# Performance work log

Measured on AMD Instinct MI355X. Metric: run time of the kernel, lower is better.

Reference implementation:

```python
import jax, jax.numpy as jnp
import numpy as np
import jax.scipy.linalg as jsl

# ---- module constants (mirror __init__ buffers) ----
T0, T1, DT = 0.0, 1.0, 1e-3
DIM, NSTEPS, M, TQ, B = 8, 2048, 64, 1024, 1
DS = (T1 - T0) / NSTEPS
STEPS = jnp.linspace(T0, T1, NSTEPS + 1)            # [S+1]
ZPTS = jnp.linspace(T0 + DT * 5.5, T1 - DT * 5.5, M)  # inducing points [M]
SQRT_DS = float(np.sqrt(DS))
SQRT_DT = float(np.sqrt(DT))


def _hurst(t, y0, W1, b1, W2, b2, Wc1, bc1, Wc2, bc2, dw, cw):
    # compute_hurst: sigmoid(driving_action(t)*dw + condition_net(y0)*cw)
    tc_in = t.reshape(-1, 1)                                             # [N,1]
    feat = jnp.concatenate([jnp.sin(tc_in), jnp.cos(tc_in), tc_in], -1)  # [N,3]
    tc = jax.nn.sigmoid(jnp.tanh(feat @ W1.T + b1) @ W2.T + b2)          # [N,dim]
    pc = jax.nn.sigmoid(jnp.tanh(y0 @ Wc1.T + bc1) @ Wc2.T + bc2)        # [1,dim]
    return jax.nn.sigmoid(tc * dw + pc * cw)                             # [N,dim]


def _safe_pow(x, a):
    # x**a for x>=0, with well-defined (zero) gradient at x==0
    mask = x > 0
    xs = jnp.where(mask, x, 1.0)
    return jnp.where(mask, xs ** a, 0.0)


def _compute_weight(t, y0, params, eps=1e-12):
    # compute_weight (Muniandy et al. weight); returns [S, N, dim]
    h = _hurst(t, y0, *params)[None]                              # [1,N,dim]
    d0 = jax.nn.relu(t[None, :] - STEPS[:-1, None])[..., None]    # [S,N,1]
    d1 = jax.nn.relu(t[None, :] - STEPS[1:, None])[..., None]     # [S,N,1]
    w = jnp.sqrt(_safe_pow(d0, 2.0 * h) - _safe_pow(d1, 2.0 * h) + eps)
    w = w / jnp.sqrt(2.0 * h * DS)
    return w / jnp.exp(jax.lax.lgamma(h + 0.5))


def _increment_weight(t, y0, params):
    # increment_weight: g_i / dt (finite difference of clamped weights)
    wa = jnp.maximum(_compute_weight(t, y0, params), 0.0)
    wb = jnp.maximum(_compute_weight(t + DT, y0, params), 0.0)
    return jnp.maximum((wb - wa) * SQRT_DS / DT, 0.0)             # [S,N,dim]


def _forward(t, y0, eps_z, W1, b1, W2, b2, Wc1, bc1, Wc2, bc2, dw, cw):
    params = (W1, b1, W2, b2, Wc1, bc1, Wc2, bc2, dw, cw)
    # --- precompute (inducing points) ---
    Kz = _increment_weight(ZPTS, y0, params)                # [S,M,dim]
    Kzz = jnp.einsum('smd,skd->dmk', Kz, Kz)                # [dim,M,M]
    Lz = jnp.linalg.cholesky(Kzz + 1e-6 * jnp.eye(M, dtype=Kzz.dtype))
    delta_Bz = jnp.einsum('dmk,dkb->dmb', Lz, eps_z)        # [dim,M,B]
    # --- forward (mean / sqrt(var)*sqrt(dt)) ---
    Kt = _increment_weight(t, y0, params)                   # [S,T,dim]
    Ktz = jnp.einsum('std,smd->dtm', Kt, Kz)                # [dim,T,M]
    alpha = jax.vmap(lambda L, b: jsl.cho_solve((L, True), b))(
        Lz, jnp.swapaxes(Ktz, -1, -2))                      # [dim,M,T]
    mean = jnp.einsum('dmt,dmb->dtb', alpha, delta_Bz)      # [dim,T,B]
    Ktt = jnp.einsum('std,sud->dtu', Kt, Kt)                # [dim,T,T]
    var = Ktt - jnp.einsum('dmt,dmu->dtu', alpha, alpha)    # [dim,T,T]
    std = jnp.sqrt(jnp.maximum(var, 1e-12)) * SQRT_DT
    return mean.reshape(-1, DIM), std.reshape(-1, DIM)


def setup_inputs() -> dict:
    key = jax.random.key(0)
    ks = jax.random.split(key, 12)
    return {
        't': jax.random.uniform(ks[0], (TQ,), jnp.float32, T0 + 0.05, T1 - 0.05),
        'y0': jax.random.normal(ks[1], (1, 1), jnp.float32),
        'eps_z': jax.random.normal(ks[2], (DIM, M, B), jnp.float32),
        'W1': jax.random.normal(ks[3], (10, 3), jnp.float32) * 0.3,
        'b1': jax.random.normal(ks[4], (10,), jnp.float32) * 0.1,
        'W2': jax.random.normal(ks[5], (DIM, 10), jnp.float32) * 0.3,
        'b2': jax.random.normal(ks[6], (DIM,), jnp.float32) * 0.1,
        'Wc1': jax.random.normal(ks[7], (10, 1), jnp.float32) * 0.3,
        'bc1': jax.random.normal(ks[8], (10,), jnp.float32) * 0.1,
        'Wc2': jax.random.normal(ks[9], (DIM, 10), jnp.float32) * 0.3,
        'bc2': jax.random.normal(ks[10], (DIM,), jnp.float32) * 0.1,
        'dw': jnp.array([0.5], jnp.float32),
        'cw': jnp.array([0.5], jnp.float32),
    }


def reference(t, y0, eps_z, W1, b1, W2, b2, Wc1, bc1, Wc2, bc2, dw, cw):
    return _forward(t, y0, eps_z, W1, b1, W2, b2, Wc1, bc1, Wc2, bc2, dw, cw)
```

## Files before the change

kernel.cpp:

```cpp
#include <hip/hip_runtime.h>
#include <cmath>

#define DIMN 8
#define SSTEPS 2048
#define MZ 64
#define TQN 1024
#define DS_F    4.8828125e-4f
#define DT_F    1.0e-3f
#define SCALE_F 22.09708691207961f
#define SQRTDT_F 0.031622776601683794f
#define LN2_F   0.6931471805599453f

typedef _Float16 f16x8 __attribute__((ext_vector_type(8)));
typedef float f32x4 __attribute__((ext_vector_type(4)));

__device__ __forceinline__ float sigmoidf_(float x) { return 1.f / (1.f + expf(-x)); }

__device__ __forceinline__ void gl_lds16(const _Float16* g, _Float16* l)
{
    __builtin_amdgcn_global_load_lds(
        (const __attribute__((address_space(1))) unsigned int*)g,
        (__attribute__((address_space(3))) unsigned int*)l, 16, 0, 0);
}

__global__ void coef_kernel(const float* __restrict__ t_in, const float* __restrict__ y0,
                            const float* __restrict__ W1, const float* __restrict__ b1,
                            const float* __restrict__ W2, const float* __restrict__ b2,
                            const float* __restrict__ Wc1, const float* __restrict__ bc1,
                            const float* __restrict__ Wc2, const float* __restrict__ bc2,
                            const float* __restrict__ dw, const float* __restrict__ cw,
                            float4* __restrict__ coef_t, float4* __restrict__ coef_z,
                            float* __restrict__ times_z)
{
    int gid = blockIdx.x * blockDim.x + threadIdx.x;
    if (gid >= TQN + MZ) return;
    bool isz = gid >= TQN;
    float tv;
    if (!isz) {
        tv = t_in[gid];
    } else {
        int j = gid - TQN;
        tv = 0.0055f + (float)j * (0.989f / 63.0f);
        times_z[j] = tv;
    }
    float y = y0[0];
    float hc[10];
    #pragma unroll
    for (int j = 0; j < 10; ++j) hc[j] = tanhf(y * Wc1[j] + bc1[j]);
    float pc[DIMN];
    #pragma unroll
    for (int d = 0; d < DIMN; ++d) {
        float s = bc2[d];
        #pragma unroll
        for (int j = 0; j < 10; ++j) s += hc[j] * Wc2[d * 10 + j];
        pc[d] = sigmoidf_(s);
    }
    float dww = dw[0], cww = cw[0];
    float4 outv[DIMN];
    for (int which = 0; which < 2; ++which) {
        float tt = (which == 0) ? tv : tv + DT_F;
        float st = sinf(tt), ct = cosf(tt);
        float hid[10];
        #pragma unroll
        for (int j = 0; j < 10; ++j)
            hid[j] = tanhf(st * W1[j * 3 + 0] + ct * W1[j * 3 + 1] + tt * W1[j * 3 + 2] + b1[j]);
        #pragma unroll
        for (int d = 0; d < DIMN; ++d) {
            float s = b2[d];
            #pragma unroll
            for (int j = 0; j < 10; ++j) s += hid[j] * W2[d * 10 + j];
            float tc = sigmoidf_(s);
            float h = sigmoidf_(tc * dww + pc[d] * cww);
            float e = 2.f * h;
            float c = rsqrtf(e * DS_F) / tgammaf(h + 0.5f);
            if (which == 0) { outv[d].x = e; outv[d].y = c; }
            else            { outv[d].z = e; outv[d].w = c; }
        }
    }
    float4* dst = isz ? (coef_z + (size_t)(gid - TQN) * DIMN) : (coef_t + (size_t)gid * DIMN);
    #pragma unroll
    for (int d = 0; d < DIMN; ++d) dst[d] = outv[d];
}

__device__ __forceinline__ void side_weights(float tt, float e, float c, int sbase,
                                             float (&w)[8])
{
    float xprev = tt - (float)sbase * DS_F;
    float pa = 0.f;
    if (xprev > 0.f) pa = __builtin_amdgcn_exp2f(e * __builtin_amdgcn_logf(xprev));
    #pragma unroll
    for (int k = 1; k <= 8; ++k) {
        float xk = tt - (float)(sbase + k) * DS_F;
        float D, pan;
        if (xk > 0.f) {
            float om = xk * __builtin_amdgcn_rcpf(xprev);
            float y2 = e * __builtin_amdgcn_logf(om);
            float wl = y2 * LN2_F;
            float em = wl * (1.f + wl * (0.5f + wl * (0.16666667f + wl * (0.041666668f + wl * 0.008333334f))));
            float g = -em;
            if (wl < -0.3f) g = 1.f - __builtin_amdgcn_exp2f(y2);
            D = pa * g;
            pan = pa - D;
        } else {
            D = pa;
            pan = 0.f;
        }
        w[k - 1] = __builtin_amdgcn_sqrtf(D + 1e-12f) * c;
        pa = pan;
        xprev = xk;
    }
}

__device__ __forceinline__ unsigned pack_hl(float v)
{
    _Float16 h = (_Float16)v;
    _Float16 l = (_Float16)(v - (float)h);
    unsigned short hu = __builtin_bit_cast(unsigned short, h);
    unsigned short lu = __builtin_bit_cast(unsigned short, l);
    return (unsigned)hu | ((unsigned)lu << 16);
}

__global__ __launch_bounds__(256) void kmat_t_kernel(const float* __restrict__ times,
                                                     const float4* __restrict__ coef,
                                                     _Float16* __restrict__ KThi,
                                                     _Float16* __restrict__ KTlo)
{
    int tid = threadIdx.x;
    int txx = tid & 31, sidx = tid >> 5;
    int t = blockIdx.x * 32 + txx;
    int sbase = blockIdx.y * 64 + sidx * 8;
    int d = blockIdx.z;
    __shared__ unsigned shhl[32][65];
    float tq = times[t];
    float4 cf = coef[(size_t)t * DIMN + d];
    float wa[8], wb[8];
    side_weights(tq,        cf.x, cf.y, sbase, wa);
    side_weights(tq + DT_F, cf.z, cf.w, sbase, wb);
    #pragma unroll
    for (int k = 0; k < 8; ++k) {
        float v = fmaxf(wb[k] - wa[k], 0.f) * SCALE_F;
        shhl[txx][sidx * 8 + k] = pack_hl(v);
    }
    __syncthreads();
    int tl = tid >> 3, sc = tid & 7;
    unsigned dwv[8];
    #pragma unroll
    for (int j = 0; j < 8; ++j) dwv[j] = shhl[tl][sc * 8 + j];
    uint4 hv, lv;
    hv.x = __builtin_amdgcn_perm(dwv[1], dwv[0], 0x05040100u);
    hv.y = __builtin_amdgcn_perm(dwv[3], dwv[2], 0x05040100u);
    hv.z = __builtin_amdgcn_perm(dwv[5], dwv[4], 0x05040100u);
    hv.w = __builtin_amdgcn_perm(dwv[7], dwv[6], 0x05040100u);
    lv.x = __builtin_amdgcn_perm(dwv[1], dwv[0], 0x07060302u);
    lv.y = __builtin_amdgcn_perm(dwv[3], dwv[2], 0x07060302u);
    lv.z = __builtin_amdgcn_perm(dwv[5], dwv[4], 0x07060302u);
    lv.w = __builtin_amdgcn_perm(dwv[7], dwv[6], 0x07060302u);
    size_t o = ((size_t)(d * 1024) + blockIdx.x * 32 + tl) * 2048 + blockIdx.y * 64 + sc * 8;
    *(uint4*)&KThi[o] = hv;
    *(uint4*)&KTlo[o] = lv;
}

__global__ __launch_bounds__(256) void kmat_z_kernel(const float* __restrict__ times,
                                                     const float4* __restrict__ coef,
                                                     float* __restrict__ Kz,
                                                     _Float16* __restrict__ KzThi,
                                                     _Float16* __restrict__ KzTlo)
{
    int tid = threadIdx.x;
    int txx = tid & 31, sidx = tid >> 5;
    int m = blockIdx.x * 32 + txx;
    int sbase = blockIdx.y * 64 + sidx * 8;
    int d = blockIdx.z;
    __shared__ unsigned shhl[32][65];
    float tq = times[m];
    float4 cf = coef[(size_t)m * DIMN + d];
    float wa[8], wb[8];
    side_weights(tq,        cf.x, cf.y, sbase, wa);
    side_weights(tq + DT_F, cf.z, cf.w, sbase, wb);
    #pragma unroll
    for (int k = 0; k < 8; ++k) {
        float v = fmaxf(wb[k] - wa[k], 0.f) * SCALE_F;
        Kz[((size_t)d * SSTEPS + sbase + k) * 64 + m] = v;
        shhl[txx][sidx * 8 + k] = pack_hl(v);
    }
    __syncthreads();
    int tl = tid >> 3, sc = tid & 7;
    unsigned dwv[8];
    #pragma unroll
    for (int j = 0; j < 8; ++j) dwv[j] = shhl[tl][sc * 8 + j];
    uint4 hv, lv;
    hv.x = __builtin_amdgcn_perm(dwv[1], dwv[0], 0x05040100u);
    hv.y = __builtin_amdgcn_perm(dwv[3], dwv[2], 0x05040100u);
    hv.z = __builtin_amdgcn_perm(dwv[5], dwv[4], 0x05040100u);
    hv.w = __builtin_amdgcn_perm(dwv[7], dwv[6], 0x05040100u);
    lv.x = __builtin_amdgcn_perm(dwv[1], dwv[0], 0x07060302u);
    lv.y = __builtin_amdgcn_perm(dwv[3], dwv[2], 0x07060302u);
    lv.z = __builtin_amdgcn_perm(dwv[5], dwv[4], 0x07060302u);
    lv.w = __builtin_amdgcn_perm(dwv[7], dwv[6], 0x07060302u);
    size_t o = ((size_t)(d * 64) + blockIdx.x * 32 + tl) * 2048 + blockIdx.y * 64 + sc * 8;
    *(uint4*)&KzThi[o] = hv;
    *(uint4*)&KzTlo[o] = lv;
}

__global__ __launch_bounds__(256) void kzz_partial_kernel(const float* __restrict__ Kz,
                                                          float* __restrict__ part)
{
    int kidx = blockIdx.x;
    int d = blockIdx.y;
    int tid = threadIdx.x, tx = tid & 15, ty = tid >> 4;
    __shared__ float As[32][64];
    float acc[4][4] = {};
    const float* base = Kz + ((size_t)d * SSTEPS + (size_t)kidx * 256) * 64;
    for (int c = 0; c < 8; ++c) {
        __syncthreads();
        #pragma unroll
        for (int l = 0; l < 2; ++l) {
            int idx = tid + l * 256;
            int r = idx >> 4, c4 = idx & 15;
            *(float4*)&As[r][c4 * 4] = *(const float4*)(base + (size_t)(c * 32 + r) * 64 + c4 * 4);
        }
        __syncthreads();
        #pragma unroll
        for (int k = 0; k < 32; ++k) {
            float av[4], bv[4];
            *(float4*)&av[0] = *(float4*)&As[k][ty * 4];
            *(float4*)&bv[0] = *(float4*)&As[k][tx * 4];
            #pragma unroll
            for (int i = 0; i < 4; ++i)
                #pragma unroll
                for (int j = 0; j < 4; ++j) acc[i][j] += av[i] * bv[j];
        }
    }
    float* dst = part + (size_t)(kidx * DIMN + d) * 4096;
    #pragma unroll
    for (int i = 0; i < 4; ++i)
        *(float4*)&dst[(size_t)(ty * 4 + i) * 64 + tx * 4] =
            make_float4(acc[i][0], acc[i][1], acc[i][2], acc[i][3]);
}

__global__ void reduce_kernel(const float* __restrict__ in, float* __restrict__ out,
                              int n, int parts)
{
    int i = blockIdx.x * 256 + threadIdx.x;
    if (i >= n) return;
    float s = 0.f;
    for (int p = 0; p < parts; ++p) s += in[(size_t)p * n + i];
    out[i] = s;
}

__global__ __launch_bounds__(64) void chol_kernel(const float* __restrict__ Kzz,
                                                  const float* __restrict__ eps_z,
                                                  float* __restrict__ Lz, float* __restrict__ dBz)
{
    int d = blockIdx.x, i = threadIdx.x;
    __shared__ float A[64][65];
    for (int r = 0; r < 64; ++r)
        A[r][i] = Kzz[(size_t)d * 4096 + (size_t)r * 64 + i] + ((r == i) ? 1e-6f : 0.f);
    __syncthreads();
    for (int j = 0; j < 64; ++j) {
        float s = 0.f;
        if (i >= j) {
            s = A[i][j];
            for (int k = 0; k < j; ++k) s -= A[i][k] * A[j][k];
        }
        __syncthreads();
        if (i == j) A[j][j] = sqrtf(fmaxf(s, 1e-30f));
        __syncthreads();
        if (i > j) A[i][j] = s / A[j][j];
        __syncthreads();
    }
    for (int r = 0; r < 64; ++r)
        Lz[(size_t)d * 4096 + (size_t)r * 64 + i] = (i <= r) ? A[r][i] : 0.f;
    float s = 0.f;
    for (int k = 0; k <= i; ++k) s += A[i][k] * eps_z[d * 64 + k];
    dBz[d * 64 + i] = s;
}

__global__ __launch_bounds__(256, 2) void ktz_mfma_kernel(const _Float16* __restrict__ KThi,
                                                          const _Float16* __restrict__ KTlo,
                                                          const _Float16* __restrict__ KzThi,
                                                          const _Float16* __restrict__ KzTlo,
                                                          float* __restrict__ part)
{
    int tid = threadIdx.x;
    int wave = tid >> 6, lane = tid & 63;
    int n = lane & 15, q = lane >> 4;
    int lr = lane >> 2, lc = (lane & 3) * 8;
    int d = blockIdx.x;
    int t0 = blockIdx.y * 128;
    int split = blockIdx.z;
    int wr = (wave >> 1) * 64, wc = (wave & 1) * 32;

    __shared__ _Float16 Ah[2][128][32], Al[2][128][32];
    __shared__ _Float16 Bh[2][64][32],  Bl[2][64][32];

    f32x4 acc[4][2];
    #pragma unroll
    for (int i = 0; i < 4; ++i)
        #pragma unroll
        for (int j = 0; j < 2; ++j) acc[i][j] = (f32x4)0.f;

    const size_t aRow = (size_t)(d * 1024 + t0);
    const size_t bRow = (size_t)(d * 64);
    int segA = wave * 32;
    int segB = wave * 16;

    auto stage = [&](int buf, int c) {
        int s0 = split * 512 + c * 32;
        size_t ga = (aRow + segA + lr) * 2048 + s0 + lc;
        size_t gb = (bRow + segB + lr) * 2048 + s0 + lc;
        gl_lds16(KThi + ga,               &Ah[buf][segA][0]);
        gl_lds16(KThi + ga + 16 * 2048,   &Ah[buf][segA + 16][0]);
        gl_lds16(KTlo + ga,               &Al[buf][segA][0]);
        gl_lds16(KTlo + ga + 16 * 2048,   &Al[buf][segA + 16][0]);
        gl_lds16(KzThi + gb,              &Bh[buf][segB][0]);
        gl_lds16(KzTlo + gb,              &Bl[buf][segB][0]);
    };

    stage(0, 0);
    __syncthreads();
    for (int c = 0; c < 16; ++c) {
        int buf = c & 1;
        if (c + 1 < 16) stage(buf ^ 1, c + 1);
        f16x8 fAh[4], fAl[4], fBh[2], fBl[2];
        #pragma unroll
        for (int i = 0; i < 4; ++i) {
            fAh[i] = *(f16x8*)&Ah[buf][wr + i * 16 + n][q * 8];
            fAl[i] = *(f16x8*)&Al[buf][wr + i * 16 + n][q * 8];
        }
        #pragma unroll
        for (int j = 0; j < 2; ++j) {
            fBh[j] = *(f16x8*)&Bh[buf][wc + j * 16 + n][q * 8];
            fBl[j] = *(f16x8*)&Bl[buf][wc + j * 16 + n][q * 8];
        }
        #pragma unroll
        for (int i = 0; i < 4; ++i)
            #pragma unroll
            for (int j = 0; j < 2; ++j) {
                acc[i][j] = __builtin_amdgcn_mfma_f32_16x16x32_f16(fAh[i], fBh[j], acc[i][j], 0, 0, 0);
                acc[i][j] = __builtin_amdgcn_mfma_f32_16x16x32_f16(fAh[i], fBl[j], acc[i][j], 0, 0, 0);
                acc[i][j] = __builtin_amdgcn_mfma_f32_16x16x32_f16(fAl[i], fBh[j], acc[i][j], 0, 0, 0);
            }
        __syncthreads();
    }
    float* dst = part + ((size_t)(split * DIMN + d)) * 1024 * 64;
    #pragma unroll
    for (int i = 0; i < 4; ++i)
        #pragma unroll
        for (int j = 0; j < 2; ++j)
            #pragma unroll
            for (int r = 0; r < 4; ++r) {
                int t = t0 + wr + i * 16 + q * 4 + r;
                dst[(size_t)t * 64 + wc + j * 16 + n] = acc[i][j][r];
            }
}

__global__ __launch_bounds__(64) void solve_kernel(const float* __restrict__ Lz,
                                                   const float* __restrict__ part2,
                                                   const float* __restrict__ dBz,
                                                   _Float16* __restrict__ aPhi,
                                                   _Float16* __restrict__ aPlo,
                                                   _Float16* __restrict__ aNhi,
                                                   _Float16* __restrict__ aNlo,
                                                   float* __restrict__ out0)
{
    int d = blockIdx.y;
    int t0 = blockIdx.x * 64;
    int i = threadIdx.x;
    __shared__ float L[64][65];
    __shared__ float bL[64][65];
    __shared__ float inv[64];
    __shared__ float dB[64];
    for (int r = 0; r < 64; ++r)
        L[r][i] = Lz[(size_t)d * 4096 + (size_t)r * 64 + i];
    dB[i] = dBz[d * 64 + i];
    for (int r = 0; r < 64; ++r) {
        size_t base = ((size_t)d * 1024 + t0 + r) * 64 + i;
        float s = part2[base] + part2[base + 524288] + part2[base + 1048576] + part2[base + 1572864];
        bL[i][r] = s;
    }
    __syncthreads();
    inv[i] = 1.f / L[i][i];
    __syncthreads();
    for (int j = 0; j < 64; ++j) {
        float s = bL[j][i];
        for (int k = 0; k < j; ++k) s -= L[j][k] * bL[k][i];
        bL[j][i] = s * inv[j];
    }
    for (int j = 63; j >= 0; --j) {
        float s = bL[j][i];
        for (int k = j + 1; k < 64; ++k) s -= L[k][j] * bL[k][i];
        bL[j][i] = s * inv[j];
    }
    float mn = 0.f;
    for (int m = 0; m < 64; ++m) mn += bL[m][i] * dB[m];
    out0[d * 1024 + t0 + i] = mn;
    size_t o = ((size_t)(d * 1024 + t0 + i)) * 64;
    for (int g = 0; g < 8; ++g) {
        union { _Float16 h[8]; float4 v; } ph, pl, nh, nl;
        #pragma unroll
        for (int k = 0; k < 8; ++k) {
            float x = bL[g * 8 + k][i];
            _Float16 h = (_Float16)x;
            _Float16 lo = (_Float16)(x - (float)h);
            ph.h[k] = h;  pl.h[k] = lo;
            nh.h[k] = -h; nl.h[k] = -lo;
        }
        *(float4*)&aPhi[o + g * 8] = ph.v;
        *(float4*)&aPlo[o + g * 8] = pl.v;
        *(float4*)&aNhi[o + g * 8] = nh.v;
        *(float4*)&aNlo[o + g * 8] = nl.v;
    }
}

__global__ __launch_bounds__(256, 2) void var_mfma_kernel(const _Float16* __restrict__ KThi,
                                                          const _Float16* __restrict__ KTlo,
                                                          const _Float16* __restrict__ aPhi,
                                                          const _Float16* __restrict__ aPlo,
                                                          const _Float16* __restrict__ aNhi,
                                                          const _Float16* __restrict__ aNlo,
                                                          float* __restrict__ out1)
{
    int tid = threadIdx.x;
    int wave = tid >> 6, lane = tid & 63;
    int n = lane & 15, q = lane >> 4;
    int lr = lane >> 2, lc = (lane & 3) * 8;
    int d = blockIdx.x;
    int t0 = blockIdx.y * 128, u0 = blockIdx.z * 128;
    int wr = (wave >> 1) * 64, wc = (wave & 1) * 64;

    __shared__ _Float16 Ah[2][128][32], Al[2][128][32], Bh[2][128][32], Bl[2][128][32];

    f32x4 acc[4][4];
    #pragma unroll
    for (int i = 0; i < 4; ++i)
        #pragma unroll
        for (int j = 0; j < 4; ++j) acc[i][j] = (f32x4)0.f;

    const size_t aRow = (size_t)(d * 1024 + t0);
    const size_t bRow = (size_t)(d * 1024 + u0);
    int segA = wave * 32;

    auto stage = [&](int buf, int ck) {
        const _Float16 *ph, *pl, *qh, *ql;
        size_t str; int col;
        if (ck < 64) { ph = KThi; pl = KTlo; qh = KThi; ql = KTlo; str = 2048; col = ck * 32; }
        else         { ph = aPhi; pl = aPlo; qh = aNhi; ql = aNlo; str = 64;  col = (ck - 64) * 32; }
        size_t ga = (aRow + segA + lr) * str + col + lc;
        size_t gb = (bRow + segA + lr) * str + col + lc;
        gl_lds16(ph + ga,            &Ah[buf][segA][0]);
        gl_lds16(ph + ga + 16 * str, &Ah[buf][segA + 16][0]);
        gl_lds16(pl + ga,            &Al[buf][segA][0]);
        gl_lds16(pl + ga + 16 * str, &Al[buf][segA + 16][0]);
        gl_lds16(qh + gb,            &Bh[buf][segA][0]);
        gl_lds16(qh + gb + 16 * str, &Bh[buf][segA + 16][0]);
        gl_lds16(ql + gb,            &Bl[buf][segA][0]);
        gl_lds16(ql + gb + 16 * str, &Bl[buf][segA + 16][0]);
    };

    stage(0, 0);
    __syncthreads();
    for (int ck = 0; ck < 66; ++ck) {
        int buf = ck & 1;
        if (ck + 1 < 66) stage(buf ^ 1, ck + 1);
        f16x8 fAh[4], fAl[4], fBh[4], fBl[4];
        #pragma unroll
        for (int i = 0; i < 4; ++i) {
            fAh[i] = *(f16x8*)&Ah[buf][wr + i * 16 + n][q * 8];
            fAl[i] = *(f16x8*)&Al[buf][wr + i * 16 + n][q * 8];
            fBh[i] = *(f16x8*)&Bh[buf][wc + i * 16 + n][q * 8];
            fBl[i] = *(f16x8*)&Bl[buf][wc + i * 16 + n][q * 8];
        }
        #pragma unroll
        for (int i = 0; i < 4; ++i)
            #pragma unroll
            for (int j = 0; j < 4; ++j) {
                acc[i][j] = __builtin_amdgcn_mfma_f32_16x16x32_f16(fAh[i], fBh[j], acc[i][j], 0, 0, 0);
                acc[i][j] = __builtin_amdgcn_mfma_f32_16x16x32_f16(fAh[i], fBl[j], acc[i][j], 0, 0, 0);
                acc[i][j] = __builtin_amdgcn_mfma_f32_16x16x32_f16(fAl[i], fBh[j], acc[i][j], 0, 0, 0);
            }
        __syncthreads();
    }
    float* dst = out1 + ((size_t)d << 20);
    #pragma unroll
    for (int i = 0; i < 4; ++i)
        #pragma unroll
        for (int j = 0; j < 4; ++j)
            #pragma unroll
            for (int r = 0; r < 4; ++r) {
                int t = t0 + wr + i * 16 + q * 4 + r;
                int u = u0 + wc + j * 16 + n;
                float v = acc[i][j][r];
                dst[(size_t)t * 1024 + u] = sqrtf(fmaxf(v, 1e-12f)) * SQRTDT_F;
            }
}

extern "C" void kernel_launch(void* const* d_in, const int* in_sizes, int n_in,
                              void* d_out, int out_size, void* d_ws, size_t ws_size,
                              hipStream_t stream)
{
    const float* t_in  = (const float*)d_in[0];
    const float* y0    = (const float*)d_in[1];
    const float* eps_z = (const float*)d_in[2];
    const float* W1    = (const float*)d_in[3];
    const float* b1    = (const float*)d_in[4];
    const float* W2    = (const float*)d_in[5];
    const float* b2    = (const float*)d_in[6];
    const float* Wc1   = (const float*)d_in[7];
    const float* bc1   = (const float*)d_in[8];
    const float* Wc2   = (const float*)d_in[9];
    const float* bc2   = (const float*)d_in[10];
    const float* dw    = (const float*)d_in[11];
    const float* cw    = (const float*)d_in[12];

    float* ws = (float*)d_ws;
    size_t off = 0;
    auto carve = [&](size_t n) { float* p = ws + off; off += n; return p; };
    float* coef_t   = carve(32768);
    float* coef_z   = carve(2048);
    float* times_z  = carve(64);
    float* Kzz      = carve(32768);
    float* Lz       = carve(32768);
    float* dBz      = carve(512);
    float* Kz       = carve(1048576);
    _Float16* KThi  = (_Float16*)carve(8388608);
    _Float16* KTlo  = (_Float16*)carve(8388608);
    _Float16* KzThi = (_Float16*)carve(524288);
    _Float16* KzTlo = (_Float16*)carve(524288);
    float* part1    = carve(262144);
    float* part2    = carve(2097152);
    _Float16* aPhi  = (_Float16*)carve(262144);
    _Float16* aPlo  = (_Float16*)carve(262144);
    _Float16* aNhi  = (_Float16*)carve(262144);
    _Float16* aNlo  = (_Float16*)carve(262144);

    float* out0 = (float*)d_out;
    float* out1 = out0 + (size_t)DIMN * 1024;

    coef_kernel<<<9, 128, 0, stream>>>(t_in, y0, W1, b1, W2, b2, Wc1, bc1, Wc2, bc2, dw, cw,
                                       (float4*)coef_t, (float4*)coef_z, times_z);
    kmat_t_kernel<<<dim3(32, 32, 8), 256, 0, stream>>>(t_in, (const float4*)coef_t,
                                                       KThi, KTlo);
    kmat_z_kernel<<<dim3(2, 32, 8), 256, 0, stream>>>(times_z, (const float4*)coef_z,
                                                      Kz, KzThi, KzTlo);
    kzz_partial_kernel<<<dim3(8, 8), 256, 0, stream>>>(Kz, part1);
    reduce_kernel<<<128, 256, 0, stream>>>(part1, Kzz, 32768, 8);
    chol_kernel<<<8, 64, 0, stream>>>(Kzz, eps_z, Lz, dBz);
    ktz_mfma_kernel<<<dim3(8, 8, 4), 256, 0, stream>>>(KThi, KTlo, KzThi, KzTlo, part2);
    solve_kernel<<<dim3(16, 8), 64, 0, stream>>>(Lz, part2, dBz, aPhi, aPlo, aNhi, aNlo, out0);
    var_mfma_kernel<<<dim3(8, 8, 8), 256, 0, stream>>>(KThi, KTlo, aPhi, aPlo, aNhi, aNlo, out1);
}
```

Measured before the change: 385.9 us.

## Exploit symmetry of variance matrix and swizzle LDS layout in var kernel

```diff
diff --git a/kernel.cpp b/kernel.cpp
--- a/kernel.cpp
+++ b/kernel.cpp
@@ -413,7 +413,7 @@
     }
 }
 
-__global__ __launch_bounds__(256, 2) void var_mfma_kernel(const _Float16* __restrict__ KThi,
+__global__ __launch_bounds__(128, 2) void var_mfma_kernel(const _Float16* __restrict__ KThi,
                                                           const _Float16* __restrict__ KTlo,
                                                           const _Float16* __restrict__ aPhi,
                                                           const _Float16* __restrict__ aPlo,
@@ -424,12 +424,18 @@
     int tid = threadIdx.x;
     int wave = tid >> 6, lane = tid & 63;
     int n = lane & 15, q = lane >> 4;
-    int lr = lane >> 2, lc = (lane & 3) * 8;
+    int lr = lane >> 2;
+    int lcs = (((lane & 3) ^ ((lr >> 1) & 3)) * 8);
+    int qs  = ((q ^ ((n >> 1) & 3)) * 8);
     int d = blockIdx.x;
-    int t0 = blockIdx.y * 128, u0 = blockIdx.z * 128;
-    int wr = (wave >> 1) * 64, wc = (wave & 1) * 64;
-
-    __shared__ _Float16 Ah[2][128][32], Al[2][128][32], Bh[2][128][32], Bl[2][128][32];
+    int ti = 0, rem = blockIdx.y;
+    while (rem >= 16 - 2 * ti) { rem -= 16 - 2 * ti; ++ti; }
+    int uj = 2 * ti + rem;
+    int t0 = ti * 128, u0 = uj * 64;
+    int wr = wave * 64;
+
+    __shared__ _Float16 Ah[2][128][32], Al[2][128][32];
+    __shared__ _Float16 Bh[2][64][32],  Bl[2][64][32];
 
     f32x4 acc[4][4];
     #pragma unroll
@@ -439,23 +445,28 @@
 
     const size_t aRow = (size_t)(d * 1024 + t0);
     const size_t bRow = (size_t)(d * 1024 + u0);
-    int segA = wave * 32;
+    int segA = wave * 64;
+    int segB = wave * 32;
 
     auto stage = [&](int buf, int ck) {
         const _Float16 *ph, *pl, *qh, *ql;
         size_t str; int col;
         if (ck < 64) { ph = KThi; pl = KTlo; qh = KThi; ql = KTlo; str = 2048; col = ck * 32; }
         else         { ph = aPhi; pl = aPlo; qh = aNhi; ql = aNlo; str = 64;  col = (ck - 64) * 32; }
-        size_t ga = (aRow + segA + lr) * str + col + lc;
-        size_t gb = (bRow + segA + lr) * str + col + lc;
+        size_t ga = (aRow + segA + lr) * str + col + lcs;
+        size_t gb = (bRow + segB + lr) * str + col + lcs;
         gl_lds16(ph + ga,            &Ah[buf][segA][0]);
         gl_lds16(ph + ga + 16 * str, &Ah[buf][segA + 16][0]);
+        gl_lds16(ph + ga + 32 * str, &Ah[buf][segA + 32][0]);
+        gl_lds16(ph + ga + 48 * str, &Ah[buf][segA + 48][0]);
         gl_lds16(pl + ga,            &Al[buf][segA][0]);
         gl_lds16(pl + ga + 16 * str, &Al[buf][segA + 16][0]);
-        gl_lds16(qh + gb,            &Bh[buf][segA][0]);
-        gl_lds16(qh + gb + 16 * str, &Bh[buf][segA + 16][0]);
-        gl_lds16(ql + gb,            &Bl[buf][segA][0]);
-        gl_lds16(ql + gb + 16 * str, &Bl[buf][segA + 16][0]);
+        gl_lds16(pl + ga + 32 * str, &Al[buf][segA + 32][0]);
+        gl_lds16(pl + ga + 48 * str, &Al[buf][segA + 48][0]);
+        gl_lds16(qh + gb,            &Bh[buf][segB][0]);
+        gl_lds16(qh + gb + 16 * str, &Bh[buf][segB + 16][0]);
+        gl_lds16(ql + gb,            &Bl[buf][segB][0]);
+        gl_lds16(ql + gb + 16 * str, &Bl[buf][segB + 16][0]);
     };
 
     stage(0, 0);
@@ -466,10 +477,10 @@
         f16x8 fAh[4], fAl[4], fBh[4], fBl[4];
         #pragma unroll
         for (int i = 0; i < 4; ++i) {
-            fAh[i] = *(f16x8*)&Ah[buf][wr + i * 16 + n][q * 8];
-            fAl[i] = *(f16x8*)&Al[buf][wr + i * 16 + n][q * 8];
-            fBh[i] = *(f16x8*)&Bh[buf][wc + i * 16 + n][q * 8];
-            fBl[i] = *(f16x8*)&Bl[buf][wc + i * 16 + n][q * 8];
+            fAh[i] = *(f16x8*)&Ah[buf][wr + i * 16 + n][qs];
+            fAl[i] = *(f16x8*)&Al[buf][wr + i * 16 + n][qs];
+            fBh[i] = *(f16x8*)&Bh[buf][i * 16 + n][qs];
+            fBl[i] = *(f16x8*)&Bl[buf][i * 16 + n][qs];
         }
         #pragma unroll
         for (int i = 0; i < 4; ++i)
@@ -482,17 +493,36 @@
         __syncthreads();
     }
     float* dst = out1 + ((size_t)d << 20);
-    #pragma unroll
-    for (int i = 0; i < 4; ++i)
-        #pragma unroll
-        for (int j = 0; j < 4; ++j)
+    int tw0 = t0 + wr;
+    bool above = (u0 >= tw0 + 64);
+    bool below = (u0 + 64 <= tw0);
+    if (!below) {
+        #pragma unroll
+        for (int i = 0; i < 4; ++i) {
+            int tb = tw0 + i * 16 + q * 4;
             #pragma unroll
-            for (int r = 0; r < 4; ++r) {
-                int t = t0 + wr + i * 16 + q * 4 + r;
-                int u = u0 + wc + j * 16 + n;
-                float v = acc[i][j][r];
-                dst[(size_t)t * 1024 + u] = sqrtf(fmaxf(v, 1e-12f)) * SQRTDT_F;
+            for (int j = 0; j < 4; ++j) {
+                int u = u0 + j * 16 + n;
+                float fv[4];
+                #pragma unroll
+                for (int r = 0; r < 4; ++r)
+                    fv[r] = sqrtf(fmaxf(acc[i][j][r], 1e-12f)) * SQRTDT_F;
+                if (above) {
+                    #pragma unroll
+                    for (int r = 0; r < 4; ++r)
+                        dst[(size_t)(tb + r) * 1024 + u] = fv[r];
+                    *(float4*)&dst[(size_t)u * 1024 + tb] = make_float4(fv[0], fv[1], fv[2], fv[3]);
+                } else {
+                    #pragma unroll
+                    for (int r = 0; r < 4; ++r) {
+                        int t = tb + r;
+                        if (u >= t) dst[(size_t)t * 1024 + u] = fv[r];
+                        if (u > t)  dst[(size_t)u * 1024 + t] = fv[r];
+                    }
+                }
             }
+        }
+    }
 }
 
 extern "C" void kernel_launch(void* const* d_in, const int* in_sizes, int n_in,
@@ -548,5 +578,5 @@
     chol_kernel<<<8, 64, 0, stream>>>(Kzz, eps_z, Lz, dBz);
     ktz_mfma_kernel<<<dim3(8, 8, 4), 256, 0, stream>>>(KThi, KTlo, KzThi, KzTlo, part2);
     solve_kernel<<<dim3(16, 8), 64, 0, stream>>>(Lz, part2, dBz, aPhi, aPlo, aNhi, aNlo, out0);
-    var_mfma_kernel<<<dim3(8, 8, 8), 256, 0, stream>>>(KThi, KTlo, aPhi, aPlo, aNhi, aNlo, out1);
-}
+    var_mfma_kernel<<<dim3(8, 72), 128, 0, stream>>>(KThi, KTlo, aPhi, aPlo, aNhi, aNlo, out1);
+}
```

Result: no change. 389.0 us (+0.8%).
